# Kernel optimization log

Hardware: AMD Instinct MI355X
Metric: run time of the kernel (lower is better)

Reference implementation:

```python
import jax, jax.numpy as jnp
from jax import lax
import numpy as np

B, T, I, H, L, O = 64, 1024, 64, 512, 3, 1


def setup_inputs() -> dict:
    key = jax.random.key(0)
    ks = jax.random.split(key, 16)
    s_in = 1.0 / np.sqrt(H)  # PyTorch nn.RNN init scale
    inp = {
        "input": jax.random.normal(ks[0], (B, T, I), jnp.float32),
        "hidden": jnp.zeros((L, B, H), jnp.float32),
        "w_ih0": jax.random.normal(ks[1], (H, I), jnp.float32) * s_in,
        "w_hh0": jax.random.normal(ks[2], (H, H), jnp.float32) * s_in,
        "b_ih0": jax.random.normal(ks[3], (H,), jnp.float32) * s_in,
        "b_hh0": jax.random.normal(ks[4], (H,), jnp.float32) * s_in,
        "w_ih1": jax.random.normal(ks[5], (H, H), jnp.float32) * s_in,
        "w_hh1": jax.random.normal(ks[6], (H, H), jnp.float32) * s_in,
        "b_ih1": jax.random.normal(ks[7], (H,), jnp.float32) * s_in,
        "b_hh1": jax.random.normal(ks[8], (H,), jnp.float32) * s_in,
        "w_ih2": jax.random.normal(ks[9], (H, H), jnp.float32) * s_in,
        "w_hh2": jax.random.normal(ks[10], (H, H), jnp.float32) * s_in,
        "b_ih2": jax.random.normal(ks[11], (H,), jnp.float32) * s_in,
        "b_hh2": jax.random.normal(ks[12], (H,), jnp.float32) * s_in,
        "fc_w": jax.random.normal(ks[13], (O, H), jnp.float32) * s_in,
        "fc_b": jax.random.normal(ks[14], (O,), jnp.float32) * s_in,
    }
    return inp


def _rnn_layer(x, h0, w_ih, w_hh, b_ih, b_hh):
    # x: [B,T,F]; precompute the input projection for all timesteps at once.
    xp = jnp.einsum('btf,hf->bth', x, w_ih) + b_ih + b_hh  # [B,T,H]
    def step(h, xt):  # h: [B,H], xt: [B,H]
        h = jnp.tanh(xt + h @ w_hh.T)
        return h, h
    hT, ys = lax.scan(step, h0, jnp.swapaxes(xp, 0, 1))  # scan over time
    return jnp.swapaxes(ys, 0, 1), hT  # [B,T,H], [B,H]


def reference(input, hidden, w_ih0, w_hh0, b_ih0, b_hh0,
              w_ih1, w_hh1, b_ih1, b_hh1,
              w_ih2, w_hh2, b_ih2, b_hh2, fc_w, fc_b):
    layers = [(w_ih0, w_hh0, b_ih0, b_hh0),
              (w_ih1, w_hh1, b_ih1, b_hh1),
              (w_ih2, w_hh2, b_ih2, b_hh2)]
    x = input
    h_finals = []
    for l, (w_ih, w_hh, b_ih, b_hh) in enumerate(layers):
        x, hT = _rnn_layer(x, hidden[l], w_ih, w_hh, b_ih, b_hh)
        h_finals.append(hT)
    out = jnp.einsum('bth,oh->bto', x, fc_w) + fc_b  # linear head
    return out, jnp.stack(h_finals, axis=0)
```

## Files before the change

kernel.cpp:

```cpp
#include <hip/hip_runtime.h>
#include <cstddef>

#define B_ 64
#define T_ 1024
#define I_ 64
#define H_ 512
#define TC 256
#define NCHUNK (T_ / TC)
#define MTOT (B_ * T_)
#define BH (B_ * H_)
#define MC (B_ * TC)

typedef unsigned long long u64;

__device__ __forceinline__ float fast_tanh(float x) {
  float e = __builtin_amdgcn_exp2f(2.885390081777927f * x);
  float r = __builtin_amdgcn_rcpf(e + 1.0f);
  return 1.0f - 2.0f * r;
}

__device__ __forceinline__ u64 pack_h(float h, unsigned tag) {
  return ((u64)tag << 32) | (u64)__float_as_uint(h);
}

__global__ __launch_bounds__(256) void init_kernel(const float* __restrict__ hidden,
                                                   u64* __restrict__ hx) {
  int idx = blockIdx.x * 256 + threadIdx.x;
  int l = idx / BH, r = idx - l * BH;
  u64 w = pack_h(hidden[idx], 0u);
  __hip_atomic_store(&hx[((size_t)l * 2 + 1) * BH + r], w,
                     __ATOMIC_RELAXED, __HIP_MEMORY_SCOPE_AGENT);
}

__global__ __launch_bounds__(256) void gemm_xp(const float* __restrict__ A, long bstride, int K,
                                               const float* __restrict__ W,
                                               const float* __restrict__ bih,
                                               const float* __restrict__ bhh,
                                               float* __restrict__ C) {
  __shared__ float As[16][132];
  __shared__ float Ws[16][132];
  const int tid = threadIdx.x;
  const int m0 = blockIdx.y * 128, n0 = blockIdx.x * 128;
  const int tx = tid & 15, ty = tid >> 4;
  float acc[8][8] = {};
  for (int k0 = 0; k0 < K; k0 += 16) {
#pragma unroll
    for (int i = 0; i < 2; i++) {
      int idx = i * 256 + tid;
      int r = idx >> 2, kq = (idx & 3) * 4;
      int row = m0 + r;
      const float* ap = A + (long)(row >> 8) * bstride + (long)(row & 255) * K + k0 + kq;
      float4 av = *(const float4*)ap;
      As[kq + 0][r] = av.x; As[kq + 1][r] = av.y; As[kq + 2][r] = av.z; As[kq + 3][r] = av.w;
      const float* wp = W + (long)(n0 + r) * K + k0 + kq;
      float4 wv = *(const float4*)wp;
      Ws[kq + 0][r] = wv.x; Ws[kq + 1][r] = wv.y; Ws[kq + 2][r] = wv.z; Ws[kq + 3][r] = wv.w;
    }
    __syncthreads();
#pragma unroll
    for (int kk = 0; kk < 16; kk++) {
      float a[8], b[8];
      *(float4*)&a[0] = *(const float4*)&As[kk][ty * 8];
      *(float4*)&a[4] = *(const float4*)&As[kk][ty * 8 + 4];
      *(float4*)&b[0] = *(const float4*)&Ws[kk][tx * 8];
      *(float4*)&b[4] = *(const float4*)&Ws[kk][tx * 8 + 4];
#pragma unroll
      for (int i = 0; i < 8; i++)
#pragma unroll
        for (int j = 0; j < 8; j++) acc[i][j] = fmaf(a[i], b[j], acc[i][j]);
    }
    __syncthreads();
  }
#pragma unroll
  for (int i = 0; i < 8; i++) {
    int m = m0 + ty * 8 + i;
    float* cp = C + (long)m * H_ + n0 + tx * 8;
#pragma unroll
    for (int jq = 0; jq < 2; jq++) {
      int n = n0 + tx * 8 + jq * 4;
      float4 o;
      o.x = acc[i][jq * 4 + 0] + bih[n + 0] + bhh[n + 0];
      o.y = acc[i][jq * 4 + 1] + bih[n + 1] + bhh[n + 1];
      o.z = acc[i][jq * 4 + 2] + bih[n + 2] + bhh[n + 2];
      o.w = acc[i][jq * 4 + 3] + bih[n + 3] + bhh[n + 3];
      *(float4*)(cp + jq * 4) = o;
    }
  }
}

__global__ __launch_bounds__(512, 2) void rnn_scan(
    float* __restrict__ xp,
    int write_y, int is_last,
    const float* __restrict__ w_hh,
    u64* __restrict__ hx,
    float* __restrict__ hT,
    const float* __restrict__ fc_w,
    const float* __restrict__ fc_b,
    float* __restrict__ outh,
    int t0) {
  const int tid = threadIdx.x;
  const int b = blockIdx.x >> 2, q = blockIdx.x & 3;
  const int ks = tid & 31, cg = tid >> 5;
  const int k0 = ks * 16;
  const int c0 = q * 128 + cg * 8;

  float w[8][16];
#pragma unroll
  for (int j = 0; j < 8; j++) {
    const float* wp = w_hh + (long)(c0 + j) * H_ + k0;
#pragma unroll
    for (int v = 0; v < 4; v++) {
      float4 t4 = *(const float4*)(wp + v * 4);
      w[j][v * 4 + 0] = t4.x; w[j][v * 4 + 1] = t4.y;
      w[j][v * 4 + 2] = t4.z; w[j][v * 4 + 3] = t4.w;
    }
  }
  float fw[8];
  if (is_last) {
#pragma unroll
    for (int j = 0; j < 8; j++) fw[j] = fc_w[c0 + j];
  }
  __shared__ float h_lds[2][544];
  __shared__ float hp[16];

  u64* poll_base = hx + (size_t)b * H_ + tid;

  for (int trel = 0; trel < TC; trel++) {
    const int t = t0 + trel;
    const int p = trel & 1;

    float* xpp = xp + ((long)b * TC + trel) * H_ + c0;
    float4 x0 = *(const float4*)xpp;
    float4 x1 = *(const float4*)(xpp + 4);

    {
      u64* pw = poll_base + (size_t)((t & 1) ^ 1) * BH;
      u64 wv = __hip_atomic_load(pw, __ATOMIC_RELAXED, __HIP_MEMORY_SCOPE_AGENT);
      while ((unsigned)(wv >> 32) != (unsigned)t) {
        __builtin_amdgcn_s_sleep(1);
        wv = __hip_atomic_load(pw, __ATOMIC_RELAXED, __HIP_MEMORY_SCOPE_AGENT);
      }
      h_lds[p][tid + (tid >> 4)] = __uint_as_float((unsigned)wv);
    }
    __syncthreads();

    float hk[16];
    {
      const float* hl = &h_lds[p][k0 + ks];
#pragma unroll
      for (int kk = 0; kk < 16; kk++) hk[kk] = hl[kk];
    }

    float acc[8] = {0.f, 0.f, 0.f, 0.f, 0.f, 0.f, 0.f, 0.f};
#pragma unroll
    for (int kk = 0; kk < 16; kk++)
#pragma unroll
      for (int j = 0; j < 8; j++) acc[j] = fmaf(hk[kk], w[j][kk], acc[j]);

#pragma unroll
    for (int m = 1; m < 32; m <<= 1)
#pragma unroll
      for (int j = 0; j < 8; j++) acc[j] += __shfl_xor(acc[j], m, 64);

    float hv[8];
    hv[0] = fast_tanh(acc[0] + x0.x); hv[1] = fast_tanh(acc[1] + x0.y);
    hv[2] = fast_tanh(acc[2] + x0.z); hv[3] = fast_tanh(acc[3] + x0.w);
    hv[4] = fast_tanh(acc[4] + x1.x); hv[5] = fast_tanh(acc[5] + x1.y);
    hv[6] = fast_tanh(acc[6] + x1.z); hv[7] = fast_tanh(acc[7] + x1.w);

    if (ks < 8) {
      u64 wv = pack_h(hv[ks], (unsigned)(t + 1));
      __hip_atomic_store(hx + (size_t)(t & 1) * BH + (size_t)b * H_ + c0 + ks, wv,
                         __ATOMIC_RELAXED, __HIP_MEMORY_SCOPE_AGENT);
    }

    if (ks == 0) {
      float4 o0 = make_float4(hv[0], hv[1], hv[2], hv[3]);
      float4 o1 = make_float4(hv[4], hv[5], hv[6], hv[7]);
      if (write_y) { *(float4*)xpp = o0; *(float4*)(xpp + 4) = o1; }
      if (t == T_ - 1) {
        float* hp2 = hT + (long)b * H_ + c0;
        *(float4*)hp2 = o0; *(float4*)(hp2 + 4) = o1;
      }
      if (is_last) {
        float pacc = 0.f;
#pragma unroll
        for (int j = 0; j < 8; j++) pacc = fmaf(hv[j], fw[j], pacc);
        hp[cg] = pacc;
      }
    }
    if (is_last) {
      __syncthreads();
      if (tid == 0) {
        float s = 0.f;
#pragma unroll
        for (int i = 0; i < 16; i++) s += hp[i];
        if (q == 0) s += fc_b[0];
        atomicAdd(outh + (long)b * T_ + t, s);
      }
    }
  }
}

extern "C" void kernel_launch(void* const* d_in, const int* in_sizes, int n_in,
                              void* d_out, int out_size, void* d_ws, size_t ws_size,
                              hipStream_t stream) {
  const float* input  = (const float*)d_in[0];
  const float* hidden = (const float*)d_in[1];
  const float* w_ih0 = (const float*)d_in[2];
  const float* w_hh0 = (const float*)d_in[3];
  const float* b_ih0 = (const float*)d_in[4];
  const float* b_hh0 = (const float*)d_in[5];
  const float* w_ih1 = (const float*)d_in[6];
  const float* w_hh1 = (const float*)d_in[7];
  const float* b_ih1 = (const float*)d_in[8];
  const float* b_hh1 = (const float*)d_in[9];
  const float* w_ih2 = (const float*)d_in[10];
  const float* w_hh2 = (const float*)d_in[11];
  const float* b_ih2 = (const float*)d_in[12];
  const float* b_hh2 = (const float*)d_in[13];
  const float* fc_w  = (const float*)d_in[14];
  const float* fc_b  = (const float*)d_in[15];

  float* out = (float*)d_out;
  float* hT  = out + MTOT;

  char* ws = (char*)d_ws;
  u64* hx = (u64*)ws;
  float* bufA = (float*)(ws + (4 << 20));
  float* bufB = bufA + (size_t)MC * H_;

  hipMemsetAsync(out, 0, (size_t)MTOT * sizeof(float), stream);
  init_kernel<<<dim3(384), dim3(256), 0, stream>>>(hidden, hx);

  dim3 gthr(256), ggrid(H_ / 128, MC / 128);
  dim3 sthr(512), sgrid(256);

  const size_t HX = 2 * (size_t)BH;

  for (int c = 0; c < NCHUNK; c++) {
    int t0 = c * TC;
    gemm_xp<<<ggrid, gthr, 0, stream>>>(input + (long)t0 * I_, (long)T_ * I_, I_,
                                        w_ih0, b_ih0, b_hh0, bufA);
    rnn_scan<<<sgrid, sthr, 0, stream>>>(bufA, 1, 0, w_hh0, hx + 0 * HX,
                                         hT + 0 * BH, fc_w, fc_b, out, t0);
    gemm_xp<<<ggrid, gthr, 0, stream>>>(bufA, (long)TC * H_, H_,
                                        w_ih1, b_ih1, b_hh1, bufB);
    rnn_scan<<<sgrid, sthr, 0, stream>>>(bufB, 1, 0, w_hh1, hx + 1 * HX,
                                         hT + 1 * BH, fc_w, fc_b, out, t0);
    gemm_xp<<<ggrid, gthr, 0, stream>>>(bufB, (long)TC * H_, H_,
                                        w_ih2, b_ih2, b_hh2, bufA);
    rnn_scan<<<sgrid, sthr, 0, stream>>>(bufA, 0, 1, w_hh2, hx + 2 * HX,
                                         hT + 2 * BH, fc_w, fc_b, out, t0);
  }
}
```

Baseline: 8.411 ms.

## Double scan block threads to 1024 and use packed FMA for recurrent matvec

Each scan workgroup now has 1024 threads, and each 32-lane group handles 4 output columns instead of 8. The per-thread recurrent weights are held as float2 pairs so the matvec can use packed FMA. The LDS layout is padded to match the new float2 reads. This halves the serial per-step work and register pressure per thread, but adds more waves per CU and a larger workgroup barrier at each timestep. All 256 blocks must still be co-resident for the spin-wait handoff to avoid deadlock.

New measurement: 8.349 ms. About the same (-0.7%).

```diff
diff --git a/kernel.cpp b/kernel.cpp
--- a/kernel.cpp
+++ b/kernel.cpp
@@ -12,6 +12,15 @@
 #define MC (B_ * TC)
 
 typedef unsigned long long u64;
+typedef float f2 __attribute__((ext_vector_type(2)));
+
+__device__ __forceinline__ f2 pk_fma(f2 a, f2 b, f2 c) {
+#if __has_builtin(__builtin_elementwise_fma)
+  return __builtin_elementwise_fma(a, b, c);
+#else
+  f2 r; r.x = fmaf(a.x, b.x, c.x); r.y = fmaf(a.y, b.y, c.y); return r;
+#endif
+}
 
 __device__ __forceinline__ float fast_tanh(float x) {
   float e = __builtin_amdgcn_exp2f(2.885390081777927f * x);
@@ -88,7 +97,7 @@
   }
 }
 
-__global__ __launch_bounds__(512, 2) void rnn_scan(
+__global__ __launch_bounds__(1024, 4) void rnn_scan(
     float* __restrict__ xp,
     int write_y, int is_last,
     const float* __restrict__ w_hh,
@@ -102,26 +111,23 @@
   const int b = blockIdx.x >> 2, q = blockIdx.x & 3;
   const int ks = tid & 31, cg = tid >> 5;
   const int k0 = ks * 16;
-  const int c0 = q * 128 + cg * 8;
-
-  float w[8][16];
-#pragma unroll
-  for (int j = 0; j < 8; j++) {
-    const float* wp = w_hh + (long)(c0 + j) * H_ + k0;
-#pragma unroll
-    for (int v = 0; v < 4; v++) {
-      float4 t4 = *(const float4*)(wp + v * 4);
-      w[j][v * 4 + 0] = t4.x; w[j][v * 4 + 1] = t4.y;
-      w[j][v * 4 + 2] = t4.z; w[j][v * 4 + 3] = t4.w;
-    }
-  }
-  float fw[8];
+  const int c0 = q * 128 + cg * 4;
+
+  f2 w2[4][8];
+#pragma unroll
+  for (int j = 0; j < 4; j++) {
+    const f2* wp2 = (const f2*)(w_hh + (long)(c0 + j) * H_ + k0);
+#pragma unroll
+    for (int i = 0; i < 8; i++) w2[j][i] = wp2[i];
+  }
+  float fw[4];
   if (is_last) {
 #pragma unroll
-    for (int j = 0; j < 8; j++) fw[j] = fc_w[c0 + j];
-  }
-  __shared__ float h_lds[2][544];
-  __shared__ float hp[16];
+    for (int j = 0; j < 4; j++) fw[j] = fc_w[c0 + j];
+  }
+
+  __shared__ float h_lds[2][576];
+  __shared__ float hp[32];
 
   u64* poll_base = hx + (size_t)b * H_ + tid;
 
@@ -130,63 +136,64 @@
     const int p = trel & 1;
 
     float* xpp = xp + ((long)b * TC + trel) * H_ + c0;
-    float4 x0 = *(const float4*)xpp;
-    float4 x1 = *(const float4*)(xpp + 4);
-
-    {
+    float4 x4 = *(const float4*)xpp;
+
+    if (tid < 512) {
       u64* pw = poll_base + (size_t)((t & 1) ^ 1) * BH;
       u64 wv = __hip_atomic_load(pw, __ATOMIC_RELAXED, __HIP_MEMORY_SCOPE_AGENT);
       while ((unsigned)(wv >> 32) != (unsigned)t) {
         __builtin_amdgcn_s_sleep(1);
         wv = __hip_atomic_load(pw, __ATOMIC_RELAXED, __HIP_MEMORY_SCOPE_AGENT);
       }
-      h_lds[p][tid + (tid >> 4)] = __uint_as_float((unsigned)wv);
+      h_lds[p][tid + (tid >> 4) * 2] = __uint_as_float((unsigned)wv);
     }
     __syncthreads();
 
-    float hk[16];
+    f2 hk2[8];
     {
-      const float* hl = &h_lds[p][k0 + ks];
-#pragma unroll
-      for (int kk = 0; kk < 16; kk++) hk[kk] = hl[kk];
-    }
-
-    float acc[8] = {0.f, 0.f, 0.f, 0.f, 0.f, 0.f, 0.f, 0.f};
-#pragma unroll
-    for (int kk = 0; kk < 16; kk++)
-#pragma unroll
-      for (int j = 0; j < 8; j++) acc[j] = fmaf(hk[kk], w[j][kk], acc[j]);
+      const f2* hl = (const f2*)&h_lds[p][ks * 18];
+#pragma unroll
+      for (int i = 0; i < 8; i++) hk2[i] = hl[i];
+    }
+
+    f2 acc2[4];
+#pragma unroll
+    for (int j = 0; j < 4; j++) acc2[j] = (f2){0.f, 0.f};
+#pragma unroll
+    for (int i = 0; i < 8; i++)
+#pragma unroll
+      for (int j = 0; j < 4; j++) acc2[j] = pk_fma(hk2[i], w2[j][i], acc2[j]);
+
+    float acc[4];
+#pragma unroll
+    for (int j = 0; j < 4; j++) acc[j] = acc2[j].x + acc2[j].y;
 
 #pragma unroll
     for (int m = 1; m < 32; m <<= 1)
 #pragma unroll
-      for (int j = 0; j < 8; j++) acc[j] += __shfl_xor(acc[j], m, 64);
-
-    float hv[8];
-    hv[0] = fast_tanh(acc[0] + x0.x); hv[1] = fast_tanh(acc[1] + x0.y);
-    hv[2] = fast_tanh(acc[2] + x0.z); hv[3] = fast_tanh(acc[3] + x0.w);
-    hv[4] = fast_tanh(acc[4] + x1.x); hv[5] = fast_tanh(acc[5] + x1.y);
-    hv[6] = fast_tanh(acc[6] + x1.z); hv[7] = fast_tanh(acc[7] + x1.w);
-
-    if (ks < 8) {
+      for (int j = 0; j < 4; j++) acc[j] += __shfl_xor(acc[j], m, 64);
+
+    float hv[4];
+    hv[0] = fast_tanh(acc[0] + x4.x);
+    hv[1] = fast_tanh(acc[1] + x4.y);
+    hv[2] = fast_tanh(acc[2] + x4.z);
+    hv[3] = fast_tanh(acc[3] + x4.w);
+
+    if (ks < 4) {
       u64 wv = pack_h(hv[ks], (unsigned)(t + 1));
       __hip_atomic_store(hx + (size_t)(t & 1) * BH + (size_t)b * H_ + c0 + ks, wv,
                          __ATOMIC_RELAXED, __HIP_MEMORY_SCOPE_AGENT);
     }
 
     if (ks == 0) {
-      float4 o0 = make_float4(hv[0], hv[1], hv[2], hv[3]);
-      float4 o1 = make_float4(hv[4], hv[5], hv[6], hv[7]);
-      if (write_y) { *(float4*)xpp = o0; *(float4*)(xpp + 4) = o1; }
-      if (t == T_ - 1) {
-        float* hp2 = hT + (long)b * H_ + c0;
-        *(float4*)hp2 = o0; *(float4*)(hp2 + 4) = o1;
-      }
+      float4 o = make_float4(hv[0], hv[1], hv[2], hv[3]);
+      if (write_y) *(float4*)xpp = o;
+      if (t == T_ - 1) *(float4*)(hT + (long)b * H_ + c0) = o;
       if (is_last) {
-        float pacc = 0.f;
-#pragma unroll
-        for (int j = 0; j < 8; j++) pacc = fmaf(hv[j], fw[j], pacc);
-        hp[cg] = pacc;
+        float pa = 0.f;
+#pragma unroll
+        for (int j = 0; j < 4; j++) pa = fmaf(hv[j], fw[j], pa);
+        hp[cg] = pa;
       }
     }
     if (is_last) {
@@ -194,7 +201,7 @@
       if (tid == 0) {
         float s = 0.f;
 #pragma unroll
-        for (int i = 0; i < 16; i++) s += hp[i];
+        for (int i = 0; i < 32; i++) s += hp[i];
         if (q == 0) s += fc_b[0];
         atomicAdd(outh + (long)b * T_ + t, s);
       }
@@ -234,7 +241,7 @@
   init_kernel<<<dim3(384), dim3(256), 0, stream>>>(hidden, hx);
 
   dim3 gthr(256), ggrid(H_ / 128, MC / 128);
-  dim3 sthr(512), sgrid(256);
+  dim3 sthr(1024), sgrid(256);
 
   const size_t HX = 2 * (size_t)BH;
 
```
